# Performance work log

Hardware: AMD Instinct MI355X
Metric: run time of the kernel (lower is better)

## Reference

```python
import jax, jax.numpy as jnp
import numpy as np

D, H, L, DFF, V = 512, 8, 6, 2048, 32000
PAD = 0

def make_pe(max_len, d):
    pos = jnp.arange(max_len, dtype=jnp.float32)[:, None]
    div = jnp.exp(jnp.arange(0, d, 2, dtype=jnp.float32) * (-np.log(10000.0) / d))
    ang = pos * div  # [max_len, d/2]
    pe = jnp.zeros((max_len, d), jnp.float32)
    pe = pe.at[:, 0::2].set(jnp.sin(ang)).at[:, 1::2].set(jnp.cos(ang))
    return pe

def layernorm(x, g, b, eps=1e-5):
    m = x.mean(-1, keepdims=True)
    v = ((x - m) ** 2).mean(-1, keepdims=True)
    return (x - m) * jax.lax.rsqrt(v + eps) * g + b

def mha(q_in, k_in, v_in, W, Bv, mask):
    # W: [4, D, D] (q,k,v,out); Bv: [4, D]; mask broadcastable to [B,H,Tq,Tk] bool
    b, sq, d = q_in.shape
    hd = d // H
    def proj(x, w, bb):
        y = x @ w + bb
        return y.reshape(x.shape[0], x.shape[1], H, hd).transpose(0, 2, 1, 3)  # bhsd
    Q, K, Vh = proj(q_in, W[0], Bv[0]), proj(k_in, W[1], Bv[1]), proj(v_in, W[2], Bv[2])
    scores = jnp.einsum('bhqd,bhkd->bhqk', Q, K) / np.sqrt(hd).astype(np.float32)
    scores = jnp.where(mask, scores, jnp.float32(-1e9))
    attn = jax.nn.softmax(scores, axis=-1)
    ctx = jnp.einsum('bhqk,bhkd->bhqd', attn, Vh).transpose(0, 2, 1, 3).reshape(b, sq, d)
    return ctx @ W[3] + Bv[3]

def ffn(x, w1, b1, w2, b2):
    return jax.nn.relu(x @ w1 + b1) @ w2 + b2

def setup_inputs() -> dict:
    key = jax.random.key(0)
    ks = jax.random.split(key, 16)
    s = 0.02
    inp = {
        'src': jax.random.randint(ks[0], (8, 512), 0, V, dtype=jnp.int32),
        'tgt': jax.random.randint(ks[1], (8, 512), 0, V, dtype=jnp.int32),
        'src_emb': (jax.random.normal(ks[2], (V, D)) * s).at[PAD].set(0.0),
        'tgt_emb': (jax.random.normal(ks[3], (V, D)) * s).at[PAD].set(0.0),
        'enc_attn_w': jax.random.normal(ks[4], (L, 4, D, D)) * s,
        'enc_attn_b': jnp.zeros((L, 4, D)),
        'enc_ffn_w1': jax.random.normal(ks[5], (L, D, DFF)) * s,
        'enc_ffn_b1': jnp.zeros((L, DFF)),
        'enc_ffn_w2': jax.random.normal(ks[6], (L, DFF, D)) * s,
        'enc_ffn_b2': jnp.zeros((L, D)),
        'enc_ln_g': jnp.ones((L, 2, D)),
        'enc_ln_b': jnp.zeros((L, 2, D)),
        'dec_self_w': jax.random.normal(ks[7], (L, 4, D, D)) * s,
        'dec_self_b': jnp.zeros((L, 4, D)),
        'dec_cross_w': jax.random.normal(ks[8], (L, 4, D, D)) * s,
        'dec_cross_b': jnp.zeros((L, 4, D)),
        'dec_ffn_w1': jax.random.normal(ks[9], (L, D, DFF)) * s,
        'dec_ffn_b1': jnp.zeros((L, DFF)),
        'dec_ffn_w2': jax.random.normal(ks[10], (L, DFF, D)) * s,
        'dec_ffn_b2': jnp.zeros((L, D)),
        'dec_ln_g': jnp.ones((L, 3, D)),
        'dec_ln_b': jnp.zeros((L, 3, D)),
        'out_w': jax.random.normal(ks[11], (D, V)) * s,
        'out_b': jnp.zeros((V,)),
    }
    return inp

def reference(src, tgt, src_emb, tgt_emb, enc_attn_w, enc_attn_b, enc_ffn_w1, enc_ffn_b1,
              enc_ffn_w2, enc_ffn_b2, enc_ln_g, enc_ln_b, dec_self_w, dec_self_b,
              dec_cross_w, dec_cross_b, dec_ffn_w1, dec_ffn_b1, dec_ffn_w2, dec_ffn_b2,
              dec_ln_g, dec_ln_b, out_w, out_b):
    B_, S = src.shape
    T = tgt.shape[1]
    pe = make_pe(max(S, T), D)
    scale = jnp.float32(np.sqrt(D))

    src_pad = (src != PAD)[:, None, None, :]                    # [B,1,1,S]
    causal = jnp.tril(jnp.ones((T, T), bool))                   # [T,T]
    tgt_mask = (tgt != PAD)[:, None, None, :] & causal[None, None]  # [B,1,T,T]

    # encoder (dropout = identity at inference)
    x = src_emb[src] * scale + pe[None, :S]
    for i in range(L):
        a = mha(x, x, x, enc_attn_w[i], enc_attn_b[i], src_pad)
        x = layernorm(x + a, enc_ln_g[i, 0], enc_ln_b[i, 0])
        f = ffn(x, enc_ffn_w1[i], enc_ffn_b1[i], enc_ffn_w2[i], enc_ffn_b2[i])
        x = layernorm(x + f, enc_ln_g[i, 1], enc_ln_b[i, 1])
    memory = x

    # decoder
    y = tgt_emb[tgt] * scale + pe[None, :T]
    for i in range(L):
        a = mha(y, y, y, dec_self_w[i], dec_self_b[i], tgt_mask)
        y = layernorm(y + a, dec_ln_g[i, 0], dec_ln_b[i, 0])
        c = mha(y, memory, memory, dec_cross_w[i], dec_cross_b[i], src_pad)
        y = layernorm(y + c, dec_ln_g[i, 1], dec_ln_b[i, 1])
        f = ffn(y, dec_ffn_w1[i], dec_ffn_b1[i], dec_ffn_w2[i], dec_ffn_b2[i])
        y = layernorm(y + f, dec_ln_g[i, 2], dec_ln_b[i, 2])

    return y @ out_w + out_b  # [B, T, tgt_vocab]
```

## Files before the change

kernel.cpp:

```cpp
#include <hip/hip_runtime.h>
#include <hip/hip_bf16.h>


#define Dm 512
#define Hh 8
#define HD 64
#define Ll 6
#define DFFv 2048
#define Vv 32000
#define Bb 8
#define Ss 512
#define NTOK (Bb * Ss)

typedef __bf16 bf16x8 __attribute__((ext_vector_type(8)));
typedef __bf16 bf16x4 __attribute__((ext_vector_type(4)));
typedef float  f32x4  __attribute__((ext_vector_type(4)));

#define GLOAD16(gp, lp) __builtin_amdgcn_global_load_lds( \
    (const __attribute__((address_space(1))) unsigned int*)(const void*)(gp), \
    (__attribute__((address_space(3))) unsigned int*)(void*)(lp), 16, 0, 0)

__global__ void embed_pe_k(const int* __restrict__ tok, const float* __restrict__ emb,
                           float* __restrict__ out, __bf16* __restrict__ outb, int Slen)
{
    int row = blockIdx.x;
    int s = row % Slen;
    int t = tok[row];
    const float* e = emb + (size_t)t * Dm;
    float* o = out + (size_t)row * Dm;
    __bf16* ob = outb + (size_t)row * Dm;
    for (int dd = threadIdx.x; dd < Dm; dd += blockDim.x) {
        int j = dd >> 1;
        float div = expf((float)(2 * j) * (-9.210340371976184f / 512.0f));
        float ang = (float)s * div;
        float pe = (dd & 1) ? cosf(ang) : sinf(ang);
        float v = e[dd] * 22.627416997969522f + pe;
        o[dd] = v;
        ob[dd] = (__bf16)v;
    }
}

__global__ __launch_bounds__(256) void wtr_k(const float* __restrict__ W,
                                             __bf16* __restrict__ Wt, int K, int N)
{
    __shared__ float t[32][33];
    size_t msz = (size_t)K * N;
    const float* Wm = W + (size_t)blockIdx.z * msz;
    __bf16* Wtm = Wt + (size_t)blockIdx.z * msz;
    int n0 = blockIdx.x * 32, k0 = blockIdx.y * 32;
    int r = threadIdx.x >> 3, c4 = (threadIdx.x & 7) * 4;
    float4 v = *reinterpret_cast<const float4*>(&Wm[(size_t)(k0 + r) * N + n0 + c4]);
    t[r][c4] = v.x; t[r][c4 + 1] = v.y; t[r][c4 + 2] = v.z; t[r][c4 + 3] = v.w;
    __syncthreads();
    int n = threadIdx.x >> 3, kq = (threadIdx.x & 7) * 4;
    bf16x4 o;
    o[0] = (__bf16)t[kq + 0][n]; o[1] = (__bf16)t[kq + 1][n];
    o[2] = (__bf16)t[kq + 2][n]; o[3] = (__bf16)t[kq + 3][n];
    *reinterpret_cast<bf16x4*>(&Wtm[(size_t)(n0 + n) * K + k0 + kq]) = o;
}

template<int BM, int BN, int RELU, int MODE>
__global__ __launch_bounds__(256) void gemm_mfma_k(const __bf16* __restrict__ A,
                                                   const __bf16* __restrict__ Wt,
                                                   const float* __restrict__ bias,
                                                   void* __restrict__ Cout,
                                                   __bf16* __restrict__ out_k,
                                                   __bf16* __restrict__ out_vT,
                                                   int M, int N, int K)
{
    constexpr int NF_M = BM / 32;
    constexpr int NF_N = BN / 32;
    __shared__ __bf16 As[BM * 32];
    __shared__ __bf16 Bs[BN * 32];
    const int tid = threadIdx.x;
    const int wave = tid >> 6, lane = tid & 63;
    const int wr = wave >> 1, wc = wave & 1;
    const int row0 = blockIdx.y * BM, col0 = blockIdx.x * BN;

    f32x4 acc[NF_M][NF_N] = {};

    const int rsub = lane >> 2;
    const int kel  = (lane & 3) * 8;
    const int fr   = lane & 15;
    const int kg   = lane >> 4;

    for (int k0 = 0; k0 < K; k0 += 32) {
        #pragma unroll
        for (int cc = 0; cc < BM / 64; ++cc) {
            int c = wave * (BM / 64) + cc;
            GLOAD16(A + (size_t)(row0 + c * 16 + rsub) * K + k0 + kel,
                    As + c * 512 + lane * 8);
        }
        #pragma unroll
        for (int cc = 0; cc < BN / 64; ++cc) {
            int c = wave * (BN / 64) + cc;
            GLOAD16(Wt + (size_t)(col0 + c * 16 + rsub) * K + k0 + kel,
                    Bs + c * 512 + lane * 8);
        }
        __syncthreads();

        const bf16x8* Av = reinterpret_cast<const bf16x8*>(As);
        const bf16x8* Bv = reinterpret_cast<const bf16x8*>(Bs);
        bf16x8 af[NF_M], bq[NF_N];
        #pragma unroll
        for (int m = 0; m < NF_M; ++m)
            af[m] = Av[(wr * (BM / 2) + m * 16 + fr) * 4 + kg];
        #pragma unroll
        for (int n = 0; n < NF_N; ++n)
            bq[n] = Bv[(wc * (BN / 2) + n * 16 + fr) * 4 + kg];
        #pragma unroll
        for (int m = 0; m < NF_M; ++m)
            #pragma unroll
            for (int n = 0; n < NF_N; ++n)
                acc[m][n] = __builtin_amdgcn_mfma_f32_16x16x32_bf16(
                    af[m], bq[n], acc[m][n], 0, 0, 0);
        __syncthreads();
    }

    #pragma unroll
    for (int m = 0; m < NF_M; ++m) {
        #pragma unroll
        for (int n = 0; n < NF_N; ++n) {
            int colg = col0 + wc * (BN / 2) + n * 16 + fr;
            float bv = bias[colg];
            #pragma unroll
            for (int j = 0; j < 4; ++j) {
                int row = row0 + wr * (BM / 2) + m * 16 + kg * 4 + j;
                float v = acc[m][n][j] + bv;
                if (RELU) v = fmaxf(v, 0.f);
                if constexpr (MODE == 0) {
                    ((float*)Cout)[(size_t)row * N + colg] = v;
                } else if constexpr (MODE == 1) {
                    ((__bf16*)Cout)[(size_t)row * N + colg] = (__bf16)v;
                } else {
                    int seg = colg >> 9;
                    int c = colg & 511;
                    bool isV = (MODE == 2) ? (seg == 2) : (seg == 1);
                    if (!isV) {
                        __bf16* o = (MODE == 2 && seg == 1) ? out_k : (__bf16*)Cout;
                        o[(size_t)row * 512 + c] = (__bf16)v;
                    } else {
                        int bi = row >> 9, s = row & 511;
                        int hh = c >> 6, f = c & 63;
                        out_vT[(size_t)((bi * 8 + hh) * 64 + f) * 512 + s] = (__bf16)v;
                    }
                }
            }
        }
    }
}

__global__ __launch_bounds__(256) void attn_mfma_k(const __bf16* __restrict__ Qb,
                                                   const __bf16* __restrict__ Kb,
                                                   const __bf16* __restrict__ VbT,
                                                   __bf16* __restrict__ Ob,
                                                   const int* __restrict__ key_tok,
                                                   int causal)
{
    __shared__ __bf16 Ks[128 * 64];
    __shared__ __bf16 Vs[64 * 128];
    __shared__ __bf16 Pl[4][16 * 128];

    const int tid = threadIdx.x;
    const int w = tid >> 6, lane = tid & 63;
    const int fr = lane & 15, kg = lane >> 4;
    const int q0 = blockIdx.x * 64;
    const int h = blockIdx.y, b = blockIdx.z;
    const int qrow = q0 + w * 16 + fr;
    const int swz = (fr & 7) << 4;

    bf16x8 qf[2];
    {
        const __bf16* qp = Qb + ((size_t)(b * 512 + qrow) * 512 + h * 64 + kg * 8);
        qf[0] = *reinterpret_cast<const bf16x8*>(qp);
        qf[1] = *reinterpret_cast<const bf16x8*>(qp + 32);
    }

    f32x4 po[4] = {};
    float m_run = -3.0e38f, l_run = 0.f;
    __bf16* pw = Pl[w];

    const int kkend = causal ? ((q0 + 64 + 127) & ~127) : 512;
    for (int kk0 = 0; kk0 < kkend; kk0 += 128) {
        #pragma unroll
        for (int c = 0; c < 4; ++c) {
            int ch = c * 256 + tid;
            int r = ch >> 3, gsk = (ch & 7) ^ (r & 7);
            GLOAD16(Kb + ((size_t)(b * 512 + kk0 + r) * 512 + h * 64 + gsk * 8),
                    Ks + ch * 8);
            int f = ch >> 4, gsv = (ch & 15) ^ (f & 7);
            GLOAD16(VbT + ((size_t)((b * 8 + h) * 64 + f) * 512 + kk0 + gsv * 8),
                    Vs + ch * 8);
        }
        __syncthreads();

        unsigned long long vm0 = __ballot(key_tok[b * 512 + kk0 + lane] != 0);
        unsigned long long vm1 = __ballot(key_tok[b * 512 + kk0 + 64 + lane] != 0);

        f32x4 st[8];
        #pragma unroll
        for (int kt = 0; kt < 8; ++kt) {
            f32x4 s = {};
            #pragma unroll
            for (int ks = 0; ks < 2; ++ks) {
                int byte = ((kt * 16 + fr) * 128 + ks * 64 + kg * 16) ^ swz;
                bf16x8 kf = *reinterpret_cast<const bf16x8*>((const char*)Ks + byte);
                s = __builtin_amdgcn_mfma_f32_16x16x32_bf16(kf, qf[ks], s, 0, 0, 0);
            }
            st[kt] = s;
        }

        float sv[8][4];
        float mloc = -3.0e38f;
        #pragma unroll
        for (int kt = 0; kt < 8; ++kt) {
            unsigned long long vm = (kt < 4) ? vm0 : vm1;
            #pragma unroll
            for (int j = 0; j < 4; ++j) {
                int kl = kt * 16 + kg * 4 + j;
                float s = st[kt][j] * 0.125f;
                bool ok = (vm >> (kl & 63)) & 1ull;
                if (causal && (kk0 + kl > qrow)) ok = false;
                s = ok ? s : -1e9f;
                sv[kt][j] = s;
                mloc = fmaxf(mloc, s);
            }
        }
        mloc = fmaxf(mloc, __shfl_xor(mloc, 16));
        mloc = fmaxf(mloc, __shfl_xor(mloc, 32));
        float m_new = fmaxf(m_run, mloc);
        float scale = __expf(m_run - m_new);
        float ls = 0.f;
        #pragma unroll
        for (int kt = 0; kt < 8; ++kt)
            #pragma unroll
            for (int j = 0; j < 4; ++j) {
                float p = __expf(sv[kt][j] - m_new);
                sv[kt][j] = p;
                ls += p;
            }
        ls += __shfl_xor(ls, 16);
        ls += __shfl_xor(ls, 32);
        l_run = l_run * scale + ls;
        m_run = m_new;

        #pragma unroll
        for (int kt = 0; kt < 8; ++kt)
            #pragma unroll
            for (int c = 0; c < 2; ++c) {
                union { __bf16 hh[2]; unsigned u; } pk;
                pk.hh[0] = (__bf16)sv[kt][2 * c];
                pk.hh[1] = (__bf16)sv[kt][2 * c + 1];
                int byte = (fr * 256 + kt * 32 + kg * 8 + c * 4) ^ swz;
                *reinterpret_cast<unsigned*>((char*)pw + byte) = pk.u;
            }

        {
            int qb4 = kg * 4;
            float s0 = __shfl(scale, qb4 + 0), s1 = __shfl(scale, qb4 + 1);
            float s2 = __shfl(scale, qb4 + 2), s3 = __shfl(scale, qb4 + 3);
            #pragma unroll
            for (int nf = 0; nf < 4; ++nf) {
                po[nf][0] *= s0; po[nf][1] *= s1;
                po[nf][2] *= s2; po[nf][3] *= s3;
            }
        }

        #pragma unroll
        for (int ks2 = 0; ks2 < 4; ++ks2) {
            int pbyte = (fr * 256 + ks2 * 64 + kg * 16) ^ swz;
            bf16x8 pa = *reinterpret_cast<const bf16x8*>((const char*)pw + pbyte);
            #pragma unroll
            for (int nf = 0; nf < 4; ++nf) {
                int vbyte = ((nf * 16 + fr) * 256 + ks2 * 64 + kg * 16) ^ swz;
                bf16x8 vf = *reinterpret_cast<const bf16x8*>((const char*)Vs + vbyte);
                po[nf] = __builtin_amdgcn_mfma_f32_16x16x32_bf16(pa, vf, po[nf], 0, 0, 0);
            }
        }
        __syncthreads();
    }

    {
        int qb4 = kg * 4;
        float r0 = 1.0f / __shfl(l_run, qb4 + 0);
        float r1 = 1.0f / __shfl(l_run, qb4 + 1);
        float r2 = 1.0f / __shfl(l_run, qb4 + 2);
        float r3 = 1.0f / __shfl(l_run, qb4 + 3);
        #pragma unroll
        for (int nf = 0; nf < 4; ++nf) {
            size_t base = (size_t)(b * 512 + q0 + w * 16 + qb4) * 512 + h * 64 + nf * 16 + fr;
            Ob[base]           = (__bf16)(po[nf][0] * r0);
            Ob[base + 512]     = (__bf16)(po[nf][1] * r1);
            Ob[base + 1024]    = (__bf16)(po[nf][2] * r2);
            Ob[base + 1536]    = (__bf16)(po[nf][3] * r3);
        }
    }
}

__global__ __launch_bounds__(256) void add_ln_k(float* __restrict__ x,
                                                const float* __restrict__ a,
                                                const float* __restrict__ g,
                                                const float* __restrict__ bb,
                                                __bf16* __restrict__ xb)
{
    int row = blockIdx.x;
    size_t base = (size_t)row * Dm;
    int tid = threadIdx.x;
    float v0 = x[base + tid]       + a[base + tid];
    float v1 = x[base + tid + 256] + a[base + tid + 256];
    float s  = v0 + v1;
    float s2 = v0 * v0 + v1 * v1;
    #pragma unroll
    for (int o = 1; o < 64; o <<= 1) {
        s  += __shfl_xor(s, o);
        s2 += __shfl_xor(s2, o);
    }
    __shared__ float red[8];
    int wid = tid >> 6, lane = tid & 63;
    if (lane == 0) { red[wid] = s; red[wid + 4] = s2; }
    __syncthreads();
    s  = red[0] + red[1] + red[2] + red[3];
    s2 = red[4] + red[5] + red[6] + red[7];
    float mean = s * (1.0f / 512.0f);
    float var  = s2 * (1.0f / 512.0f) - mean * mean;
    float rstd = rsqrtf(var + 1e-5f);
    float y0 = (v0 - mean) * rstd * g[tid]       + bb[tid];
    float y1 = (v1 - mean) * rstd * g[tid + 256] + bb[tid + 256];
    x[base + tid]        = y0;
    x[base + tid + 256]  = y1;
    xb[base + tid]       = (__bf16)y0;
    xb[base + tid + 256] = (__bf16)y1;
}

extern "C" void kernel_launch(void* const* d_in, const int* in_sizes, int n_in,
                              void* d_out, int out_size, void* d_ws, size_t ws_size,
                              hipStream_t stream)
{
    const int*   src        = (const int*)  d_in[0];
    const int*   tgt        = (const int*)  d_in[1];
    const float* src_emb    = (const float*)d_in[2];
    const float* tgt_emb    = (const float*)d_in[3];
    const float* enc_attn_w = (const float*)d_in[4];
    const float* enc_attn_b = (const float*)d_in[5];
    const float* enc_ffn_w1 = (const float*)d_in[6];
    const float* enc_ffn_b1 = (const float*)d_in[7];
    const float* enc_ffn_w2 = (const float*)d_in[8];
    const float* enc_ffn_b2 = (const float*)d_in[9];
    const float* enc_ln_g   = (const float*)d_in[10];
    const float* enc_ln_b   = (const float*)d_in[11];
    const float* dec_self_w = (const float*)d_in[12];
    const float* dec_self_b = (const float*)d_in[13];
    const float* dec_cross_w= (const float*)d_in[14];
    const float* dec_cross_b= (const float*)d_in[15];
    const float* dec_ffn_w1 = (const float*)d_in[16];
    const float* dec_ffn_b1 = (const float*)d_in[17];
    const float* dec_ffn_w2 = (const float*)d_in[18];
    const float* dec_ffn_b2 = (const float*)d_in[19];
    const float* dec_ln_g   = (const float*)d_in[20];
    const float* dec_ln_b   = (const float*)d_in[21];
    const float* out_w      = (const float*)d_in[22];
    const float* out_b      = (const float*)d_in[23];

    const size_t NROW = (size_t)NTOK * Dm;
    const size_t NH1  = (size_t)NTOK * DFFv;

    float* ws  = (float*)d_ws;
    float* xe  = ws;
    float* xd  = xe + NROW;
    float* t0  = xd + NROW;

    __bf16* xeb  = (__bf16*)(t0 + NROW);
    __bf16* xdb  = xeb + NROW;
    __bf16* qbb  = xdb + NROW;
    __bf16* kbb  = qbb + NROW;
    __bf16* vbT  = kbb + NROW;
    __bf16* ctxb = vbT + NROW;
    __bf16* h1b  = ctxb + NROW;

    const size_t WSZ  = (size_t)Dm * Dm;
    const size_t FSZ  = (size_t)Dm * DFFv;
    __bf16* w_enc_attn = h1b + NH1;
    __bf16* w_enc_f1   = w_enc_attn + 24 * WSZ;
    __bf16* w_enc_f2   = w_enc_f1 + 6 * FSZ;
    __bf16* w_dec_self = w_enc_f2 + 6 * FSZ;
    __bf16* w_dec_cross= w_dec_self + 24 * WSZ;
    __bf16* w_dec_f1   = w_dec_cross + 24 * WSZ;
    __bf16* w_dec_f2   = w_dec_f1 + 6 * FSZ;
    __bf16* w_out      = w_dec_f2 + 6 * FSZ;

    wtr_k<<<dim3(Dm / 32, Dm / 32, 24), 256, 0, stream>>>(enc_attn_w, w_enc_attn, Dm, Dm);
    wtr_k<<<dim3(DFFv / 32, Dm / 32, 6), 256, 0, stream>>>(enc_ffn_w1, w_enc_f1, Dm, DFFv);
    wtr_k<<<dim3(Dm / 32, DFFv / 32, 6), 256, 0, stream>>>(enc_ffn_w2, w_enc_f2, DFFv, Dm);
    wtr_k<<<dim3(Dm / 32, Dm / 32, 24), 256, 0, stream>>>(dec_self_w, w_dec_self, Dm, Dm);
    wtr_k<<<dim3(Dm / 32, Dm / 32, 24), 256, 0, stream>>>(dec_cross_w, w_dec_cross, Dm, Dm);
    wtr_k<<<dim3(DFFv / 32, Dm / 32, 6), 256, 0, stream>>>(dec_ffn_w1, w_dec_f1, Dm, DFFv);
    wtr_k<<<dim3(Dm / 32, DFFv / 32, 6), 256, 0, stream>>>(dec_ffn_w2, w_dec_f2, DFFv, Dm);
    wtr_k<<<dim3(Vv / 32, Dm / 32, 1), 256, 0, stream>>>(out_w, w_out, Dm, Vv);

    auto gqkv = [&](const __bf16* A, const __bf16* Wt, const float* bias) {
        gemm_mfma_k<64, 128, 0, 2><<<dim3(1536 / 128, NTOK / 64), 256, 0, stream>>>(
            A, Wt, bias, qbb, kbb, vbT, NTOK, 1536, Dm);
    };
    auto gkv = [&](const __bf16* A, const __bf16* Wt, const float* bias) {
        gemm_mfma_k<64, 128, 0, 3><<<dim3(1024 / 128, NTOK / 64), 256, 0, stream>>>(
            A, Wt, bias, kbb, nullptr, vbT, NTOK, 1024, Dm);
    };
    auto g64f = [&](const __bf16* A, const __bf16* Wt, const float* bias, float* C, int K) {
        gemm_mfma_k<64, 64, 0, 0><<<dim3(Dm / 64, NTOK / 64), 256, 0, stream>>>(
            A, Wt, bias, C, nullptr, nullptr, NTOK, Dm, K);
    };
    auto g64b = [&](const __bf16* A, const __bf16* Wt, const float* bias, __bf16* C, int K) {
        gemm_mfma_k<64, 64, 0, 1><<<dim3(Dm / 64, NTOK / 64), 256, 0, stream>>>(
            A, Wt, bias, C, nullptr, nullptr, NTOK, Dm, K);
    };
    auto attn = [&](const __bf16* Q, const __bf16* K, const __bf16* Vt, __bf16* O,
                    const int* kt, int causal) {
        attn_mfma_k<<<dim3(Ss / 64, Hh, Bb), 256, 0, stream>>>(Q, K, Vt, O, kt, causal);
    };
    auto lnorm = [&](float* x, const float* a, const float* g, const float* b, __bf16* xb) {
        add_ln_k<<<NTOK, 256, 0, stream>>>(x, a, g, b, xb);
    };

    embed_pe_k<<<NTOK, 256, 0, stream>>>(src, src_emb, xe, xeb, Ss);
    embed_pe_k<<<NTOK, 256, 0, stream>>>(tgt, tgt_emb, xd, xdb, Ss);

    for (int i = 0; i < Ll; ++i) {
        const __bf16* W = w_enc_attn + (size_t)i * 4 * WSZ;
        const float* Bv = enc_attn_b + (size_t)i * 4 * Dm;
        gqkv(xeb, W, Bv);
        attn(qbb, kbb, vbT, ctxb, src, 0);
        g64f(ctxb, W + 3 * WSZ, Bv + 3 * Dm, t0, Dm);
        lnorm(xe, t0, enc_ln_g + i * 2 * Dm, enc_ln_b + i * 2 * Dm, xeb);
        gemm_mfma_k<128, 128, 1, 1><<<dim3(DFFv / 128, NTOK / 128), 256, 0, stream>>>(
            xeb, w_enc_f1 + (size_t)i * FSZ, enc_ffn_b1 + i * DFFv, h1b, nullptr, nullptr,
            NTOK, DFFv, Dm);
        g64f(h1b, w_enc_f2 + (size_t)i * FSZ, enc_ffn_b2 + i * Dm, t0, DFFv);
        lnorm(xe, t0, enc_ln_g + i * 2 * Dm + Dm, enc_ln_b + i * 2 * Dm + Dm, xeb);
    }

    for (int i = 0; i < Ll; ++i) {
        const __bf16* Wsf = w_dec_self + (size_t)i * 4 * WSZ;
        const float* Bsf = dec_self_b + (size_t)i * 4 * Dm;
        gqkv(xdb, Wsf, Bsf);
        attn(qbb, kbb, vbT, ctxb, tgt, 1);
        g64f(ctxb, Wsf + 3 * WSZ, Bsf + 3 * Dm, t0, Dm);
        lnorm(xd, t0, dec_ln_g + i * 3 * Dm, dec_ln_b + i * 3 * Dm, xdb);

        const __bf16* Wc = w_dec_cross + (size_t)i * 4 * WSZ;
        const float* Bc = dec_cross_b + (size_t)i * 4 * Dm;
        g64b(xdb, Wc + 0 * WSZ, Bc + 0 * Dm, qbb, Dm);
        gkv(xeb, Wc + 1 * WSZ, Bc + 1 * Dm);
        attn(qbb, kbb, vbT, ctxb, src, 0);
        g64f(ctxb, Wc + 3 * WSZ, Bc + 3 * Dm, t0, Dm);
        lnorm(xd, t0, dec_ln_g + i * 3 * Dm + Dm, dec_ln_b + i * 3 * Dm + Dm, xdb);

        gemm_mfma_k<128, 128, 1, 1><<<dim3(DFFv / 128, NTOK / 128), 256, 0, stream>>>(
            xdb, w_dec_f1 + (size_t)i * FSZ, dec_ffn_b1 + i * DFFv, h1b, nullptr, nullptr,
            NTOK, DFFv, Dm);
        g64f(h1b, w_dec_f2 + (size_t)i * FSZ, dec_ffn_b2 + i * Dm, t0, DFFv);
        lnorm(xd, t0, dec_ln_g + i * 3 * Dm + 2 * Dm, dec_ln_b + i * 3 * Dm + 2 * Dm, xdb);
    }

    gemm_mfma_k<128, 256, 0, 0><<<dim3(Vv / 256, NTOK / 128), 256, 0, stream>>>(
        xdb, w_out, out_b, d_out, nullptr, nullptr, NTOK, Vv, Dm);
}
```

Before: 2.350 ms.

## Double-buffer LDS tiles in GEMM and attention; swap grid order for vocab GEMM

Gives both the GEMM and attention kernels two LDS buffers, so the next K tile (or key/value block) is issued with async global-to-LDS loads while the current tile is consumed by MFMAs. The intent is to hide global-load latency behind compute. The vocabulary projection also swaps its grid axes so consecutive blocks walk along rows, which changes how tiles are shared in L2. Costs: LDS use doubles, which can lower occupancy, and correctness depends on the barrier placement at the end of each iteration, which is not visible.

```diff
diff --git a/kernel.cpp b/kernel.cpp
--- a/kernel.cpp
+++ b/kernel.cpp
@@ -59,7 +59,7 @@
     *reinterpret_cast<bf16x4*>(&Wtm[(size_t)(n0 + n) * K + k0 + kq]) = o;
 }
 
-template<int BM, int BN, int RELU, int MODE>
+template<int BM, int BN, int RELU, int MODE, int SWAPG>
 __global__ __launch_bounds__(256) void gemm_mfma_k(const __bf16* __restrict__ A,
                                                    const __bf16* __restrict__ Wt,
                                                    const float* __restrict__ bias,
@@ -70,12 +70,13 @@
 {
     constexpr int NF_M = BM / 32;
     constexpr int NF_N = BN / 32;
-    __shared__ __bf16 As[BM * 32];
-    __shared__ __bf16 Bs[BN * 32];
+    __shared__ __bf16 As[2][BM * 32];
+    __shared__ __bf16 Bs[2][BN * 32];
     const int tid = threadIdx.x;
     const int wave = tid >> 6, lane = tid & 63;
     const int wr = wave >> 1, wc = wave & 1;
-    const int row0 = blockIdx.y * BM, col0 = blockIdx.x * BN;
+    const int row0 = (SWAPG ? blockIdx.x : blockIdx.y) * BM;
+    const int col0 = (SWAPG ? blockIdx.y : blockIdx.x) * BN;
 
     f32x4 acc[NF_M][NF_N] = {};
 
@@ -84,23 +85,31 @@
     const int fr   = lane & 15;
     const int kg   = lane >> 4;
 
-    for (int k0 = 0; k0 < K; k0 += 32) {
+    auto stage = [&](int buf, int k0) {
         #pragma unroll
         for (int cc = 0; cc < BM / 64; ++cc) {
             int c = wave * (BM / 64) + cc;
             GLOAD16(A + (size_t)(row0 + c * 16 + rsub) * K + k0 + kel,
-                    As + c * 512 + lane * 8);
+                    &As[buf][c * 512 + lane * 8]);
         }
         #pragma unroll
         for (int cc = 0; cc < BN / 64; ++cc) {
             int c = wave * (BN / 64) + cc;
             GLOAD16(Wt + (size_t)(col0 + c * 16 + rsub) * K + k0 + kel,
-                    Bs + c * 512 + lane * 8);
-        }
-        __syncthreads();
-
-        const bf16x8* Av = reinterpret_cast<const bf16x8*>(As);
-        const bf16x8* Bv = reinterpret_cast<const bf16x8*>(Bs);
+                    &Bs[buf][c * 512 + lane * 8]);
+        }
+    };
+
+    stage(0, 0);
+    __syncthreads();
+
+    const int nk = K >> 5;
+    for (int kb = 0; kb < nk; ++kb) {
+        int cur = kb & 1;
+        if (kb + 1 < nk) stage(cur ^ 1, (kb + 1) * 32);
+
+        const bf16x8* Av = reinterpret_cast<const bf16x8*>(As[cur]);
+        const bf16x8* Bv = reinterpret_cast<const bf16x8*>(Bs[cur]);
         bf16x8 af[NF_M], bq[NF_N];
         #pragma unroll
         for (int m = 0; m < NF_M; ++m)
@@ -157,8 +166,8 @@
                                                    const int* __restrict__ key_tok,
                                                    int causal)
 {
-    __shared__ __bf16 Ks[128 * 64];
-    __shared__ __bf16 Vs[64 * 128];
+    __shared__ __bf16 Ks[2][128 * 64];
+    __shared__ __bf16 Vs[2][64 * 128];
     __shared__ __bf16 Pl[4][16 * 128];
 
     const int tid = threadIdx.x;
@@ -180,19 +189,26 @@
     float m_run = -3.0e38f, l_run = 0.f;
     __bf16* pw = Pl[w];
 
-    const int kkend = causal ? ((q0 + 64 + 127) & ~127) : 512;
-    for (int kk0 = 0; kk0 < kkend; kk0 += 128) {
+    auto stage = [&](int buf, int kk0) {
         #pragma unroll
         for (int c = 0; c < 4; ++c) {
             int ch = c * 256 + tid;
             int r = ch >> 3, gsk = (ch & 7) ^ (r & 7);
             GLOAD16(Kb + ((size_t)(b * 512 + kk0 + r) * 512 + h * 64 + gsk * 8),
-                    Ks + ch * 8);
+                    &Ks[buf][ch * 8]);
             int f = ch >> 4, gsv = (ch & 15) ^ (f & 7);
             GLOAD16(VbT + ((size_t)((b * 8 + h) * 64 + f) * 512 + kk0 + gsv * 8),
-                    Vs + ch * 8);
-        }
-        __syncthreads();
+                    &Vs[buf][ch * 8]);
+        }
+    };
+
+    const int kkend = causal ? ((q0 + 64 + 127) & ~127) : 512;
+    stage(0, 0);
+    __syncthreads();
+
+    for (int kk0 = 0; kk0 < kkend; kk0 += 128) {
+        int cur = (kk0 >> 7) & 1;
+        if (kk0 + 128 < kkend) stage(cur ^ 1, kk0 + 128);
 
         unsigned long long vm0 = __ballot(key_tok[b * 512 + kk0 + lane] != 0);
         unsigned long long vm1 = __ballot(key_tok[b * 512 + kk0 + 64 + lane] != 0);
@@ -204,7 +220,7 @@
             #pragma unroll
             for (int ks = 0; ks < 2; ++ks) {
                 int byte = ((kt * 16 + fr) * 128 + ks * 64 + kg * 16) ^ swz;
-                bf16x8 kf = *reinterpret_cast<const bf16x8*>((const char*)Ks + byte);
+                bf16x8 kf = *reinterpret_cast<const bf16x8*>((const char*)Ks[cur] + byte);
                 s = __builtin_amdgcn_mfma_f32_16x16x32_bf16(kf, qf[ks], s, 0, 0, 0);
             }
             st[kt] = s;
@@ -273,7 +289,7 @@
             #pragma unroll
             for (int nf = 0; nf < 4; ++nf) {
                 int vbyte = ((nf * 16 + fr) * 256 + ks2 * 64 + kg * 16) ^ swz;
-                bf16x8 vf = *reinterpret_cast<const bf16x8*>((const char*)Vs + vbyte);
+                bf16x8 vf = *reinterpret_cast<const bf16x8*>((const char*)Vs[cur] + vbyte);
                 po[nf] = __builtin_amdgcn_mfma_f32_16x16x32_bf16(pa, vf, po[nf], 0, 0, 0);
             }
         }
@@ -398,19 +414,19 @@
     wtr_k<<<dim3(Vv / 32, Dm / 32, 1), 256, 0, stream>>>(out_w, w_out, Dm, Vv);
 
     auto gqkv = [&](const __bf16* A, const __bf16* Wt, const float* bias) {
-        gemm_mfma_k<64, 128, 0, 2><<<dim3(1536 / 128, NTOK / 64), 256, 0, stream>>>(
+        gemm_mfma_k<64, 128, 0, 2, 0><<<dim3(1536 / 128, NTOK / 64), 256, 0, stream>>>(
             A, Wt, bias, qbb, kbb, vbT, NTOK, 1536, Dm);
     };
     auto gkv = [&](const __bf16* A, const __bf16* Wt, const float* bias) {
-        gemm_mfma_k<64, 128, 0, 3><<<dim3(1024 / 128, NTOK / 64), 256, 0, stream>>>(
+        gemm_mfma_k<64, 128, 0, 3, 0><<<dim3(1024 / 128, NTOK / 64), 256, 0, stream>>>(
             A, Wt, bias, kbb, nullptr, vbT, NTOK, 1024, Dm);
     };
     auto g64f = [&](const __bf16* A, const __bf16* Wt, const float* bias, float* C, int K) {
-        gemm_mfma_k<64, 64, 0, 0><<<dim3(Dm / 64, NTOK / 64), 256, 0, stream>>>(
+        gemm_mfma_k<64, 64, 0, 0, 0><<<dim3(Dm / 64, NTOK / 64), 256, 0, stream>>>(
             A, Wt, bias, C, nullptr, nullptr, NTOK, Dm, K);
     };
     auto g64b = [&](const __bf16* A, const __bf16* Wt, const float* bias, __bf16* C, int K) {
-        gemm_mfma_k<64, 64, 0, 1><<<dim3(Dm / 64, NTOK / 64), 256, 0, stream>>>(
+        gemm_mfma_k<64, 64, 0, 1, 0><<<dim3(Dm / 64, NTOK / 64), 256, 0, stream>>>(
             A, Wt, bias, C, nullptr, nullptr, NTOK, Dm, K);
     };
     auto attn = [&](const __bf16* Q, const __bf16* K, const __bf16* Vt, __bf16* O,
@@ -431,7 +447,7 @@
         attn(qbb, kbb, vbT, ctxb, src, 0);
         g64f(ctxb, W + 3 * WSZ, Bv + 3 * Dm, t0, Dm);
         lnorm(xe, t0, enc_ln_g + i * 2 * Dm, enc_ln_b + i * 2 * Dm, xeb);
-        gemm_mfma_k<128, 128, 1, 1><<<dim3(DFFv / 128, NTOK / 128), 256, 0, stream>>>(
+        gemm_mfma_k<128, 128, 1, 1, 0><<<dim3(DFFv / 128, NTOK / 128), 256, 0, stream>>>(
             xeb, w_enc_f1 + (size_t)i * FSZ, enc_ffn_b1 + i * DFFv, h1b, nullptr, nullptr,
             NTOK, DFFv, Dm);
         g64f(h1b, w_enc_f2 + (size_t)i * FSZ, enc_ffn_b2 + i * Dm, t0, DFFv);
@@ -454,13 +470,13 @@
         g64f(ctxb, Wc + 3 * WSZ, Bc + 3 * Dm, t0, Dm);
         lnorm(xd, t0, dec_ln_g + i * 3 * Dm + Dm, dec_ln_b + i * 3 * Dm + Dm, xdb);
 
-        gemm_mfma_k<128, 128, 1, 1><<<dim3(DFFv / 128, NTOK / 128), 256, 0, stream>>>(
+        gemm_mfma_k<128, 128, 1, 1, 0><<<dim3(DFFv / 128, NTOK / 128), 256, 0, stream>>>(
             xdb, w_dec_f1 + (size_t)i * FSZ, dec_ffn_b1 + i * DFFv, h1b, nullptr, nullptr,
             NTOK, DFFv, Dm);
         g64f(h1b, w_dec_f2 + (size_t)i * FSZ, dec_ffn_b2 + i * Dm, t0, DFFv);
         lnorm(xd, t0, dec_ln_g + i * 3 * Dm + 2 * Dm, dec_ln_b + i * 3 * Dm + 2 * Dm, xdb);
     }
 
-    gemm_mfma_k<128, 256, 0, 0><<<dim3(Vv / 256, NTOK / 128), 256, 0, stream>>>(
+    gemm_mfma_k<128, 256, 0, 0, 1><<<dim3(NTOK / 128, Vv / 256), 256, 0, stream>>>(
         xdb, w_out, out_b, d_out, nullptr, nullptr, NTOK, Vv, Dm);
 }
```

Measured after the change: 2.341 ms. Within noise of the previous version (-0.4%).
